# Performance work log

Measured on AMD Instinct MI355X. Metric: run time of the kernel, lower is better.

The kernel has to match this reference:

```python
import jax, jax.numpy as jnp
import numpy as np

IN_F, OUT_F, USER_F = 1024, 512, 512
BSZ, S = 64, 256


def setup_inputs() -> dict:
    key = jax.random.key(0)
    k = jax.random.split(key, 7)
    X_doc = jax.random.normal(k[0], (BSZ, S, IN_F), dtype=jnp.float32)
    X_user = jax.random.normal(k[1], (BSZ, S, USER_F), dtype=jnp.float32)
    # xavier-normal-ish scaling for weights
    Wd = jax.random.normal(k[2], (OUT_F, IN_F), dtype=jnp.float32) * np.sqrt(2.0 / (IN_F + OUT_F))
    bd = jnp.zeros((OUT_F,), dtype=jnp.float32)
    Wu = jax.random.normal(k[3], (OUT_F, USER_F), dtype=jnp.float32) * np.sqrt(2.0 / (USER_F + OUT_F))
    bu = jnp.zeros((OUT_F,), dtype=jnp.float32)
    W = jax.random.normal(k[4], (OUT_F, OUT_F), dtype=jnp.float32) * np.sqrt(1.0 / OUT_F)
    return {"X_doc": X_doc, "X_user": X_user, "Wd": Wd, "bd": bd, "Wu": Wu, "bu": bu, "W": W}


def reference(X_doc, X_user, Wd, bd, Wu, bu, W):
    d = jnp.einsum('bsi,oi->bso', X_doc, Wd) + bd          # (b, s, out)
    u = jnp.einsum('bsi,oi->bso', X_user, Wu) + bu          # (b, s, out)
    d = d * jax.nn.sigmoid(u)
    u = u * jax.nn.sigmoid(d)
    att = jnp.tanh(jnp.einsum('bsd,de,bre->bsr', d, W, u))  # (b, s, s)
    score_d = jax.nn.softmax(att.mean(axis=2), axis=1)[..., None]  # (b, s, 1)
    score_u = jax.nn.softmax(att.mean(axis=1), axis=1)[..., None]  # (b, s, 1)
    attention_d = jnp.sum(score_d * d, axis=1)              # (b, out)
    attention_u = jnp.sum(score_u * u, axis=1)              # (b, out)
    return (attention_d, attention_u)
```

## Files before the change

### kernel.cpp

```cpp
#include <hip/hip_runtime.h>
#include <hip/hip_bf16.h>

#define S_ 256
#define BSZ_ 64
#define IN_F_ 1024
#define OUT_F_ 512
#define USER_F_ 512

typedef short short8 __attribute__((ext_vector_type(8)));
typedef float f32x4 __attribute__((ext_vector_type(4)));

__device__ __forceinline__ ushort f2bf(float f) {
  unsigned u = __float_as_uint(f);
  unsigned r = (u + 0x7FFFu + ((u >> 16) & 1u)) >> 16;
  return (ushort)r;
}
__device__ __forceinline__ float bf2f(unsigned hi16) {
  return __uint_as_float(hi16 << 16);
}
__device__ __forceinline__ float sigf(float x) {
  return 1.f / (1.f + __expf(-x));
}
__device__ __forceinline__ float tanh_safe(float x) {
  float ax = fabsf(x);
  float e = __expf(-2.f * ax);
  float r = (1.f - e) / (1.f + e);
  return copysignf(r, x);
}

__device__ __forceinline__ void gl_lds16(const ushort* g, ushort* l) {
  __builtin_amdgcn_global_load_lds(
      (const __attribute__((address_space(1))) void*)g,
      (__attribute__((address_space(3))) void*)l, 16, 0, 0);
}

__global__ void prep(const float* __restrict__ Xd, const float* __restrict__ Xu,
                     const float* __restrict__ Wd, const float* __restrict__ Wu,
                     const float* __restrict__ W,
                     ushort* __restrict__ Xd_bf, ushort* __restrict__ Xu_bf,
                     ushort* __restrict__ Wd_bf, ushort* __restrict__ Wu_bf,
                     ushort* __restrict__ Wt_bf, float* __restrict__ rowlog) {
  int i = blockIdx.x * 256 + threadIdx.x;
  if (i < 4194304) {
    float4 v = ((const float4*)Xd)[i];
    ushort4 o; o.x = f2bf(v.x); o.y = f2bf(v.y); o.z = f2bf(v.z); o.w = f2bf(v.w);
    ((ushort4*)Xd_bf)[i] = o;
  } else if (i < 6291456) {
    int j = i - 4194304;
    float4 v = ((const float4*)Xu)[j];
    ushort4 o; o.x = f2bf(v.x); o.y = f2bf(v.y); o.z = f2bf(v.z); o.w = f2bf(v.w);
    ((ushort4*)Xu_bf)[j] = o;
  } else if (i < 6422528) {
    int j = i - 6291456;
    float4 v = ((const float4*)Wd)[j];
    ushort4 o; o.x = f2bf(v.x); o.y = f2bf(v.y); o.z = f2bf(v.z); o.w = f2bf(v.w);
    ((ushort4*)Wd_bf)[j] = o;
  } else if (i < 6488064) {
    int j = i - 6422528;
    float4 v = ((const float4*)Wu)[j];
    ushort4 o; o.x = f2bf(v.x); o.y = f2bf(v.y); o.z = f2bf(v.z); o.w = f2bf(v.w);
    ((ushort4*)Wu_bf)[j] = o;
  } else if (i < 6750208) {
    int j = i - 6488064;
    Wt_bf[j] = f2bf(W[(j & 511) * 512 + (j >> 9)]);
  } else {
    int j = i - 6750208;
    ((float4*)rowlog)[j] = float4{0.f, 0.f, 0.f, 0.f};
  }
}

template <int ROWS>
__device__ __forceinline__ void stage_tile(const ushort* __restrict__ g, int K,
                                           ushort* lds, int w, int lane) {
  const int rin = lane >> 3;
  const int c = lane & 7;
#pragma unroll
  for (int i = 0; i < ROWS / 32; ++i) {
    int r = w * (ROWS / 4) + i * 8 + rin;
    int gc = c ^ (r & 7);
    gl_lds16(g + (long)r * K + gc * 8, lds + w * (ROWS / 4) * 64 + i * 512);
  }
}
__device__ __forceinline__ void stage_tile8w(const ushort* __restrict__ g, int K,
                                             ushort* lds, int w, int lane) {
  const int rin = lane >> 3, c = lane & 7;
#pragma unroll
  for (int i = 0; i < 2; ++i) {
    int r = w * 16 + i * 8 + rin;
    int gc = c ^ (r & 7);
    gl_lds16(g + (long)r * K + gc * 8, lds + w * 1024 + i * 512);
  }
}

__device__ __forceinline__ short8 frag(const ushort* lds, int row, int kk, int q) {
  int pc = (kk * 4 + q) ^ (row & 7);
  return *(const short8*)(lds + row * 64 + pc * 8);
}

__device__ __forceinline__ void compute8w(const ushort* As, const ushort* Bs,
                                          f32x4 acc[4][2], int wr, int wc,
                                          int mlane, int q) {
#pragma unroll
  for (int kk = 0; kk < 2; ++kk) {
    short8 af[4], bfr[2];
#pragma unroll
    for (int r = 0; r < 4; ++r) af[r] = frag(As, wr * 64 + r * 16 + mlane, kk, q);
#pragma unroll
    for (int c = 0; c < 2; ++c) bfr[c] = frag(Bs, wc * 32 + c * 16 + mlane, kk, q);
#pragma unroll
    for (int r = 0; r < 4; ++r)
#pragma unroll
      for (int c = 0; c < 2; ++c)
        acc[r][c] = __builtin_amdgcn_mfma_f32_16x16x32_bf16(af[r], bfr[c], acc[r][c], 0, 0, 0);
  }
}
__device__ __forceinline__ void compute4w(const ushort* As, const ushort* Bs,
                                          f32x4 acc[4][4], int wr, int wc,
                                          int mlane, int q) {
#pragma unroll
  for (int kk = 0; kk < 2; ++kk) {
    short8 af[4], bfr[4];
#pragma unroll
    for (int r = 0; r < 4; ++r) af[r] = frag(As, wr * 64 + r * 16 + mlane, kk, q);
#pragma unroll
    for (int c = 0; c < 4; ++c) bfr[c] = frag(Bs, wc * 64 + c * 16 + mlane, kk, q);
#pragma unroll
    for (int r = 0; r < 4; ++r)
#pragma unroll
      for (int c = 0; c < 4; ++c)
        acc[r][c] = __builtin_amdgcn_mfma_f32_16x16x32_bf16(af[r], bfr[c], acc[r][c], 0, 0, 0);
  }
}

#define ACC_ZERO2(a)                            \
  _Pragma("unroll") for (int r = 0; r < 4; ++r) \
  _Pragma("unroll") for (int c = 0; c < 2; ++c) { \
    a[r][c][0] = 0.f; a[r][c][1] = 0.f; a[r][c][2] = 0.f; a[r][c][3] = 0.f; }
#define ACC_ZERO4(a)                            \
  _Pragma("unroll") for (int r = 0; r < 4; ++r) \
  _Pragma("unroll") for (int c = 0; c < 4; ++c) { \
    a[r][c][0] = 0.f; a[r][c][1] = 0.f; a[r][c][2] = 0.f; a[r][c][3] = 0.f; }

__global__ __launch_bounds__(512, 4) void gemm_du(
    const ushort* __restrict__ Xd, const ushort* __restrict__ Wd,
    const float* __restrict__ bd,
    const ushort* __restrict__ Xu, const ushort* __restrict__ Wu,
    const float* __restrict__ bu,
    ushort* __restrict__ dg, ushort* __restrict__ ug) {
  __shared__ ushort sm[16384];
  ushort* As = sm; ushort* Bs = sm + 8192;
  const int i = blockIdx.x;
  const int xcd = i & 7, j = i >> 3;
  const int by = xcd * 16 + (j >> 2), bx = j & 3;
  const int tid = threadIdx.x, lane = tid & 63, w = tid >> 6;
  const int wr = w >> 2, wc = w & 3, mlane = lane & 15, q = lane >> 4;
  const int m0 = by * 128, n0 = bx * 128;

  f32x4 accd[4][2]; ACC_ZERO2(accd);
  const ushort* Ad = Xd + (long)m0 * 1024;
  const ushort* Bd = Wd + (long)n0 * 1024;
#pragma unroll 1
  for (int k = 0; k < 16; ++k) {
    stage_tile8w(Ad + k * 64, 1024, As, w, lane);
    stage_tile8w(Bd + k * 64, 1024, Bs, w, lane);
    __syncthreads();
    compute8w(As, Bs, accd, wr, wc, mlane, q);
    __syncthreads();
  }
  f32x4 accu[4][2]; ACC_ZERO2(accu);
  const ushort* Au = Xu + (long)m0 * 512;
  const ushort* Bu = Wu + (long)n0 * 512;
#pragma unroll 1
  for (int k = 0; k < 8; ++k) {
    stage_tile8w(Au + k * 64, 512, As, w, lane);
    stage_tile8w(Bu + k * 64, 512, Bs, w, lane);
    __syncthreads();
    compute8w(As, Bs, accu, wr, wc, mlane, q);
    __syncthreads();
  }

#pragma unroll
  for (int c = 0; c < 2; ++c) {
    const int gn = n0 + wc * 32 + c * 16 + mlane;
    const float bdv = bd[gn], buv = bu[gn];
#pragma unroll
    for (int r = 0; r < 4; ++r)
#pragma unroll
      for (int ii = 0; ii < 4; ++ii) {
        const int gm = m0 + wr * 64 + r * 16 + q * 4 + ii;
        const long idx = (long)gm * OUT_F_ + gn;
        float dp = accd[r][c][ii] + bdv;
        float up = accu[r][c][ii] + buv;
        float dgv = dp * sigf(up);
        float ugv = up * sigf(dgv);
        dg[idx] = f2bf(dgv);
        ug[idx] = f2bf(ugv);
      }
  }
}

__global__ __launch_bounds__(256, 3) void gemm_t(
    const ushort* __restrict__ dg, const ushort* __restrict__ Wt,
    ushort* __restrict__ t) {
  __shared__ ushort sm[16384];
  ushort* As = sm; ushort* Bs = sm + 8192;
  const int i = blockIdx.x;
  const int xcd = i & 7, j = i >> 3;
  const int by = xcd * 16 + (j >> 2), bx = j & 3;
  const int tid = threadIdx.x, lane = tid & 63, w = tid >> 6;
  const int wr = w >> 1, wc = w & 1, mlane = lane & 15, q = lane >> 4;
  const int m0 = by * 128, n0 = bx * 128;

  f32x4 acc[4][4]; ACC_ZERO4(acc);
  const ushort* A = dg + (long)m0 * 512;
  const ushort* B = Wt + (long)n0 * 512;
#pragma unroll 1
  for (int k = 0; k < 8; ++k) {
    stage_tile<128>(A + k * 64, 512, As, w, lane);
    stage_tile<128>(B + k * 64, 512, Bs, w, lane);
    __syncthreads();
    compute4w(As, Bs, acc, wr, wc, mlane, q);
    __syncthreads();
  }
#pragma unroll
  for (int c = 0; c < 4; ++c) {
    const int gn = n0 + wc * 64 + c * 16 + mlane;
#pragma unroll
    for (int r = 0; r < 4; ++r)
#pragma unroll
      for (int ii = 0; ii < 4; ++ii) {
        const int gm = m0 + wr * 64 + r * 16 + q * 4 + ii;
        t[(long)gm * OUT_F_ + gn] = f2bf(acc[r][c][ii]);
      }
  }
}

__global__ __launch_bounds__(256, 3) void att(
    const ushort* __restrict__ t, const ushort* __restrict__ ug,
    float* __restrict__ rowlog, float* __restrict__ collog) {
  __shared__ ushort sm[16384];
  ushort* As = sm; ushort* Bs = sm + 8192;
  const int i = blockIdx.x;
  const int xcd = i & 7, j = i >> 3;
  const int b = xcd * 8 + (j >> 2);
  const int mt = (j >> 1) & 1, nt = j & 1;
  const int tid = threadIdx.x, lane = tid & 63, w = tid >> 6;
  const int wr = w >> 1, wc = w & 1, mlane = lane & 15, q = lane >> 4;

  f32x4 acc[4][4]; ACC_ZERO4(acc);
  const ushort* A = t + ((long)b * S_ + mt * 128) * 512;
  const ushort* B = ug + ((long)b * S_ + nt * 128) * 512;
#pragma unroll 1
  for (int k = 0; k < 8; ++k) {
    stage_tile<128>(A + k * 64, 512, As, w, lane);
    stage_tile<128>(B + k * 64, 512, Bs, w, lane);
    __syncthreads();
    compute4w(As, Bs, acc, wr, wc, mlane, q);
    __syncthreads();
  }

  float rs[16], cs[4];
#pragma unroll
  for (int x = 0; x < 16; ++x) rs[x] = 0.f;
#pragma unroll
  for (int c = 0; c < 4; ++c) cs[c] = 0.f;
#pragma unroll
  for (int r = 0; r < 4; ++r)
#pragma unroll
    for (int c = 0; c < 4; ++c)
#pragma unroll
      for (int ii = 0; ii < 4; ++ii) {
        float v = tanh_safe(acc[r][c][ii]);
        rs[r * 4 + ii] += v;
        cs[c] += v;
      }
#pragma unroll
  for (int m = 1; m < 16; m <<= 1)
#pragma unroll
    for (int x = 0; x < 16; ++x) rs[x] += __shfl_xor(rs[x], m, 64);
#pragma unroll
  for (int m = 16; m < 64; m <<= 1)
#pragma unroll
    for (int c = 0; c < 4; ++c) cs[c] += __shfl_xor(cs[c], m, 64);

  const int s0 = mt * 128 + wr * 64;
  const int r0 = nt * 128 + wc * 64;
  if (mlane == 0) {
#pragma unroll
    for (int x = 0; x < 16; ++x)
      atomicAdd(&rowlog[b * S_ + s0 + (x >> 2) * 16 + q * 4 + (x & 3)], rs[x]);
  }
  if (q == 0) {
#pragma unroll
    for (int c = 0; c < 4; ++c)
      atomicAdd(&collog[b * S_ + r0 + c * 16 + mlane], cs[c]);
  }
}

__device__ __forceinline__ float block_max(float v, float* buf, int tid) {
  buf[tid] = v; __syncthreads();
  for (int s = 128; s > 0; s >>= 1) {
    if (tid < s) buf[tid] = fmaxf(buf[tid], buf[tid + s]);
    __syncthreads();
  }
  float r = buf[0]; __syncthreads();
  return r;
}
__device__ __forceinline__ float block_sum(float v, float* buf, int tid) {
  buf[tid] = v; __syncthreads();
  for (int s = 128; s > 0; s >>= 1) {
    if (tid < s) buf[tid] = buf[tid] + buf[tid + s];
    __syncthreads();
  }
  float r = buf[0]; __syncthreads();
  return r;
}

__global__ __launch_bounds__(256) void finalize(
    const float* __restrict__ rowlog, const float* __restrict__ collog,
    const ushort* __restrict__ dg, const ushort* __restrict__ ug,
    float* __restrict__ out) {
  __shared__ float sd[S_], su[S_], buf[S_];
  const int b = blockIdx.x >> 2, oc = blockIdx.x & 3;
  const int tid = threadIdx.x;

  const float rowmean = rowlog[b * S_ + tid] * (1.f / (float)S_);
  const float colmean = collog[b * S_ + tid] * (1.f / (float)S_);

  float md = block_max(rowmean, buf, tid);
  float ed = __expf(rowmean - md);
  float sds = block_sum(ed, buf, tid);
  sd[tid] = ed / sds;
  float mu = block_max(colmean, buf, tid);
  float eu = __expf(colmean - mu);
  float sus = block_sum(eu, buf, tid);
  su[tid] = eu / sus;
  __syncthreads();

  const int o = oc * 128 + (tid & 127);
  const ushort* src = (tid < 128) ? dg : ug;
  const float* sw = (tid < 128) ? sd : su;
  const ushort* p = src + (long)b * (S_ * OUT_F_) + o;
  float a = 0.f;
#pragma unroll 8
  for (int s = 0; s < S_; ++s) a += sw[s] * bf2f((unsigned)p[s * OUT_F_]);
  out[((tid < 128) ? 0 : BSZ_ * OUT_F_) + b * OUT_F_ + o] = a;
}

extern "C" void kernel_launch(void* const* d_in, const int* in_sizes, int n_in,
                              void* d_out, int out_size, void* d_ws, size_t ws_size,
                              hipStream_t stream) {
  (void)in_sizes; (void)n_in; (void)out_size; (void)ws_size;
  const float* Xd = (const float*)d_in[0];
  const float* Xu = (const float*)d_in[1];
  const float* Wd = (const float*)d_in[2];
  const float* bd = (const float*)d_in[3];
  const float* Wu = (const float*)d_in[4];
  const float* bu = (const float*)d_in[5];
  const float* W  = (const float*)d_in[6];
  float* out = (float*)d_out;
  char* ws = (char*)d_ws;

  ushort* Xd_bf  = (ushort*)(ws + 0L);
  ushort* Xu_bf  = (ushort*)(ws + 33554432L);
  ushort* Wd_bf  = (ushort*)(ws + 50331648L);
  ushort* Wu_bf  = (ushort*)(ws + 51380224L);
  ushort* Wt_bf  = (ushort*)(ws + 51904512L);
  ushort* dg     = (ushort*)(ws + 52428800L);
  ushort* ug     = (ushort*)(ws + 69206016L);
  float*  rowlog = (float*)(ws + 85983232L);
  float*  collog = (float*)(ws + 86048768L);
  ushort* t_buf  = Xd_bf;

  prep<<<26400, 256, 0, stream>>>(Xd, Xu, Wd, Wu, W, Xd_bf, Xu_bf,
                                  Wd_bf, Wu_bf, Wt_bf, rowlog);

  gemm_du<<<512, dim3(512), 0, stream>>>(Xd_bf, Wd_bf, bd, Xu_bf, Wu_bf, bu, dg, ug);
  gemm_t<<<512, dim3(256), 0, stream>>>(dg, Wt_bf, t_buf);
  att<<<256, dim3(256), 0, stream>>>(t_buf, ug, rowlog, collog);
  finalize<<<256, dim3(256), 0, stream>>>(rowlog, collog, dg, ug, out);
}
```

Baseline: 213.3 us.

## Double-buffer LDS in GEMM loops and reassociate bilinear form to avoid transposing W

Every GEMM main loop now uses two LDS buffers and a prefetch of the next K-tile, so loads overlap MFMA compute and one barrier per step is removed. The bilinear attention is regrouped as d·(u·W^T)^T: the middle GEMM now multiplies ug by W, whose rows can be used directly, so the prep kernel converts W with plain vectorized loads instead of the strided scalar transpose. LDS per block doubles and launch bounds drop from 3 to 2 blocks per CU for the 256-thread kernels, which lowers occupancy.

```diff
diff --git a/kernel.cpp b/kernel.cpp
--- a/kernel.cpp
+++ b/kernel.cpp
@@ -39,7 +39,7 @@
                      const float* __restrict__ W,
                      ushort* __restrict__ Xd_bf, ushort* __restrict__ Xu_bf,
                      ushort* __restrict__ Wd_bf, ushort* __restrict__ Wu_bf,
-                     ushort* __restrict__ Wt_bf, float* __restrict__ rowlog) {
+                     ushort* __restrict__ W_bf, float* __restrict__ rowlog) {
   int i = blockIdx.x * 256 + threadIdx.x;
   if (i < 4194304) {
     float4 v = ((const float4*)Xd)[i];
@@ -60,11 +60,13 @@
     float4 v = ((const float4*)Wu)[j];
     ushort4 o; o.x = f2bf(v.x); o.y = f2bf(v.y); o.z = f2bf(v.z); o.w = f2bf(v.w);
     ((ushort4*)Wu_bf)[j] = o;
-  } else if (i < 6750208) {
+  } else if (i < 6553600) {
     int j = i - 6488064;
-    Wt_bf[j] = f2bf(W[(j & 511) * 512 + (j >> 9)]);
+    float4 v = ((const float4*)W)[j];
+    ushort4 o; o.x = f2bf(v.x); o.y = f2bf(v.y); o.z = f2bf(v.z); o.w = f2bf(v.w);
+    ((ushort4*)W_bf)[j] = o;
   } else {
-    int j = i - 6750208;
+    int j = i - 6553600;
     ((float4*)rowlog)[j] = float4{0.f, 0.f, 0.f, 0.f};
   }
 }
@@ -141,14 +143,58 @@
   _Pragma("unroll") for (int c = 0; c < 4; ++c) { \
     a[r][c][0] = 0.f; a[r][c][1] = 0.f; a[r][c][2] = 0.f; a[r][c][3] = 0.f; }
 
+template <int NSTEP>
+__device__ __forceinline__ void loop8w(const ushort* __restrict__ A,
+                                       const ushort* __restrict__ B, int K,
+                                       ushort* sm, f32x4 acc[4][2], int w,
+                                       int lane, int wr, int wc, int mlane, int q) {
+  stage_tile8w(A, K, sm, w, lane);
+  stage_tile8w(B, K, sm + 8192, w, lane);
+  __syncthreads();
+  int cur = 0;
+#pragma unroll 1
+  for (int k = 0; k < NSTEP; ++k) {
+    if (k + 1 < NSTEP) {
+      ushort* dst = sm + (cur ^ 1) * 16384;
+      stage_tile8w(A + (k + 1) * 64, K, dst, w, lane);
+      stage_tile8w(B + (k + 1) * 64, K, dst + 8192, w, lane);
+    }
+    const ushort* Asc = sm + cur * 16384;
+    compute8w(Asc, Asc + 8192, acc, wr, wc, mlane, q);
+    __syncthreads();
+    cur ^= 1;
+  }
+}
+template <int NSTEP>
+__device__ __forceinline__ void loop4w(const ushort* __restrict__ A,
+                                       const ushort* __restrict__ B, int K,
+                                       ushort* sm, f32x4 acc[4][4], int w,
+                                       int lane, int wr, int wc, int mlane, int q) {
+  stage_tile<128>(A, K, sm, w, lane);
+  stage_tile<128>(B, K, sm + 8192, w, lane);
+  __syncthreads();
+  int cur = 0;
+#pragma unroll 1
+  for (int k = 0; k < NSTEP; ++k) {
+    if (k + 1 < NSTEP) {
+      ushort* dst = sm + (cur ^ 1) * 16384;
+      stage_tile<128>(A + (k + 1) * 64, K, dst, w, lane);
+      stage_tile<128>(B + (k + 1) * 64, K, dst + 8192, w, lane);
+    }
+    const ushort* Asc = sm + cur * 16384;
+    compute4w(Asc, Asc + 8192, acc, wr, wc, mlane, q);
+    __syncthreads();
+    cur ^= 1;
+  }
+}
+
 __global__ __launch_bounds__(512, 4) void gemm_du(
     const ushort* __restrict__ Xd, const ushort* __restrict__ Wd,
     const float* __restrict__ bd,
     const ushort* __restrict__ Xu, const ushort* __restrict__ Wu,
     const float* __restrict__ bu,
     ushort* __restrict__ dg, ushort* __restrict__ ug) {
-  __shared__ ushort sm[16384];
-  ushort* As = sm; ushort* Bs = sm + 8192;
+  __shared__ ushort sm[32768];
   const int i = blockIdx.x;
   const int xcd = i & 7, j = i >> 3;
   const int by = xcd * 16 + (j >> 2), bx = j & 3;
@@ -157,27 +203,11 @@
   const int m0 = by * 128, n0 = bx * 128;
 
   f32x4 accd[4][2]; ACC_ZERO2(accd);
-  const ushort* Ad = Xd + (long)m0 * 1024;
-  const ushort* Bd = Wd + (long)n0 * 1024;
-#pragma unroll 1
-  for (int k = 0; k < 16; ++k) {
-    stage_tile8w(Ad + k * 64, 1024, As, w, lane);
-    stage_tile8w(Bd + k * 64, 1024, Bs, w, lane);
-    __syncthreads();
-    compute8w(As, Bs, accd, wr, wc, mlane, q);
-    __syncthreads();
-  }
+  loop8w<16>(Xd + (long)m0 * 1024, Wd + (long)n0 * 1024, 1024, sm, accd,
+             w, lane, wr, wc, mlane, q);
   f32x4 accu[4][2]; ACC_ZERO2(accu);
-  const ushort* Au = Xu + (long)m0 * 512;
-  const ushort* Bu = Wu + (long)n0 * 512;
-#pragma unroll 1
-  for (int k = 0; k < 8; ++k) {
-    stage_tile8w(Au + k * 64, 512, As, w, lane);
-    stage_tile8w(Bu + k * 64, 512, Bs, w, lane);
-    __syncthreads();
-    compute8w(As, Bs, accu, wr, wc, mlane, q);
-    __syncthreads();
-  }
+  loop8w<8>(Xu + (long)m0 * 512, Wu + (long)n0 * 512, 512, sm, accu,
+            w, lane, wr, wc, mlane, q);
 
 #pragma unroll
   for (int c = 0; c < 2; ++c) {
@@ -199,11 +229,10 @@
   }
 }
 
-__global__ __launch_bounds__(256, 3) void gemm_t(
-    const ushort* __restrict__ dg, const ushort* __restrict__ Wt,
-    ushort* __restrict__ t) {
-  __shared__ ushort sm[16384];
-  ushort* As = sm; ushort* Bs = sm + 8192;
+__global__ __launch_bounds__(256, 2) void gemm_v(
+    const ushort* __restrict__ ug, const ushort* __restrict__ Wb,
+    ushort* __restrict__ v) {
+  __shared__ ushort sm[32768];
   const int i = blockIdx.x;
   const int xcd = i & 7, j = i >> 3;
   const int by = xcd * 16 + (j >> 2), bx = j & 3;
@@ -212,16 +241,8 @@
   const int m0 = by * 128, n0 = bx * 128;
 
   f32x4 acc[4][4]; ACC_ZERO4(acc);
-  const ushort* A = dg + (long)m0 * 512;
-  const ushort* B = Wt + (long)n0 * 512;
-#pragma unroll 1
-  for (int k = 0; k < 8; ++k) {
-    stage_tile<128>(A + k * 64, 512, As, w, lane);
-    stage_tile<128>(B + k * 64, 512, Bs, w, lane);
-    __syncthreads();
-    compute4w(As, Bs, acc, wr, wc, mlane, q);
-    __syncthreads();
-  }
+  loop4w<8>(ug + (long)m0 * 512, Wb + (long)n0 * 512, 512, sm, acc,
+            w, lane, wr, wc, mlane, q);
 #pragma unroll
   for (int c = 0; c < 4; ++c) {
     const int gn = n0 + wc * 64 + c * 16 + mlane;
@@ -230,16 +251,15 @@
 #pragma unroll
       for (int ii = 0; ii < 4; ++ii) {
         const int gm = m0 + wr * 64 + r * 16 + q * 4 + ii;
-        t[(long)gm * OUT_F_ + gn] = f2bf(acc[r][c][ii]);
+        v[(long)gm * OUT_F_ + gn] = f2bf(acc[r][c][ii]);
       }
   }
 }
 
-__global__ __launch_bounds__(256, 3) void att(
-    const ushort* __restrict__ t, const ushort* __restrict__ ug,
+__global__ __launch_bounds__(256, 2) void att(
+    const ushort* __restrict__ dgp, const ushort* __restrict__ v,
     float* __restrict__ rowlog, float* __restrict__ collog) {
-  __shared__ ushort sm[16384];
-  ushort* As = sm; ushort* Bs = sm + 8192;
+  __shared__ ushort sm[32768];
   const int i = blockIdx.x;
   const int xcd = i & 7, j = i >> 3;
   const int b = xcd * 8 + (j >> 2);
@@ -248,16 +268,9 @@
   const int wr = w >> 1, wc = w & 1, mlane = lane & 15, q = lane >> 4;
 
   f32x4 acc[4][4]; ACC_ZERO4(acc);
-  const ushort* A = t + ((long)b * S_ + mt * 128) * 512;
-  const ushort* B = ug + ((long)b * S_ + nt * 128) * 512;
-#pragma unroll 1
-  for (int k = 0; k < 8; ++k) {
-    stage_tile<128>(A + k * 64, 512, As, w, lane);
-    stage_tile<128>(B + k * 64, 512, Bs, w, lane);
-    __syncthreads();
-    compute4w(As, Bs, acc, wr, wc, mlane, q);
-    __syncthreads();
-  }
+  loop4w<8>(dgp + ((long)b * S_ + mt * 128) * 512,
+            v + ((long)b * S_ + nt * 128) * 512, 512, sm, acc,
+            w, lane, wr, wc, mlane, q);
 
   float rs[16], cs[4];
 #pragma unroll
@@ -270,9 +283,9 @@
     for (int c = 0; c < 4; ++c)
 #pragma unroll
       for (int ii = 0; ii < 4; ++ii) {
-        float v = tanh_safe(acc[r][c][ii]);
-        rs[r * 4 + ii] += v;
-        cs[c] += v;
+        float vv = tanh_safe(acc[r][c][ii]);
+        rs[r * 4 + ii] += vv;
+        cs[c] += vv;
       }
 #pragma unroll
   for (int m = 1; m < 16; m <<= 1)
@@ -365,18 +378,18 @@
   ushort* Xu_bf  = (ushort*)(ws + 33554432L);
   ushort* Wd_bf  = (ushort*)(ws + 50331648L);
   ushort* Wu_bf  = (ushort*)(ws + 51380224L);
-  ushort* Wt_bf  = (ushort*)(ws + 51904512L);
+  ushort* W_bf   = (ushort*)(ws + 51904512L);
   ushort* dg     = (ushort*)(ws + 52428800L);
   ushort* ug     = (ushort*)(ws + 69206016L);
   float*  rowlog = (float*)(ws + 85983232L);
   float*  collog = (float*)(ws + 86048768L);
-  ushort* t_buf  = Xd_bf;
-
-  prep<<<26400, 256, 0, stream>>>(Xd, Xu, Wd, Wu, W, Xd_bf, Xu_bf,
-                                  Wd_bf, Wu_bf, Wt_bf, rowlog);
+  ushort* v_buf  = Xd_bf;
+
+  prep<<<25632, 256, 0, stream>>>(Xd, Xu, Wd, Wu, W, Xd_bf, Xu_bf,
+                                  Wd_bf, Wu_bf, W_bf, rowlog);
 
   gemm_du<<<512, dim3(512), 0, stream>>>(Xd_bf, Wd_bf, bd, Xu_bf, Wu_bf, bu, dg, ug);
-  gemm_t<<<512, dim3(256), 0, stream>>>(dg, Wt_bf, t_buf);
-  att<<<256, dim3(256), 0, stream>>>(t_buf, ug, rowlog, collog);
+  gemm_v<<<512, dim3(256), 0, stream>>>(ug, W_bf, v_buf);
+  att<<<256, dim3(256), 0, stream>>>(dg, v_buf, rowlog, collog);
   finalize<<<256, dim3(256), 0, stream>>>(rowlog, collog, dg, ug, out);
 }
```

After: 210.4 us. Within noise of the previous version (-1.3%).
